# Performance work log

Hardware: AMD Instinct MI355X
Metric: run time of the kernel (lower is better)

The kernel has to match this reference:

```python
import jax, jax.numpy as jnp
import numpy as np
import math

B, C, H, W = 16, 512, 32, 32
GROUPS = 32
EPS = 1e-5


def group_norm(x, w, b):
    # x: [B, C, H, W]; normalize within each of GROUPS channel groups over (C//G, H, W)
    Bx, Cx, Hx, Wx = x.shape
    xg = x.reshape(Bx, GROUPS, Cx // GROUPS, Hx, Wx)
    mean = xg.mean(axis=(2, 3, 4), keepdims=True)
    var = xg.var(axis=(2, 3, 4), keepdims=True)
    xg = (xg - mean) * jax.lax.rsqrt(var + EPS)
    xn = xg.reshape(Bx, Cx, Hx, Wx)
    return xn * w[None, :, None, None] + b[None, :, None, None]


def setup_inputs() -> dict:
    key = jax.random.key(0)
    ks = jax.random.split(key, 4)
    x = jax.random.normal(ks[0], (B, C, H, W), dtype=jnp.float32)
    gn_w = jnp.ones((C,), dtype=jnp.float32)
    gn_b = jnp.zeros((C,), dtype=jnp.float32)
    # Conv2d 1x1 weights as [out, in] matrices; PyTorch default init scale
    qkv_w = jax.random.normal(ks[1], (3 * C, C), dtype=jnp.float32) * (1.0 / math.sqrt(C))
    qkv_b = jnp.zeros((3 * C,), dtype=jnp.float32)
    out_w = jax.random.normal(ks[2], (C, C), dtype=jnp.float32) * (1.0 / math.sqrt(C))
    out_b = jnp.zeros((C,), dtype=jnp.float32)
    return {"x": x, "gn_w": gn_w, "gn_b": gn_b, "qkv_w": qkv_w,
            "qkv_b": qkv_b, "out_w": out_w, "out_b": out_b}


def reference(x, gn_w, gn_b, qkv_w, qkv_b, out_w, out_b):
    Bx, Cx, Hx, Wx = x.shape
    N = Hx * Wx
    h = group_norm(x, gn_w, gn_b)                       # [B, C, H, W]
    hf = h.reshape(Bx, Cx, N)                           # [B, C, N]
    # 1x1 conv == channel matmul
    qkv = jnp.einsum('oc,bcn->bon', qkv_w, hf) + qkv_b[None, :, None]  # [B, 3C, N]
    q, k, v = jnp.split(qkv, 3, axis=1)                 # each [B, C, N]
    q = q.transpose(0, 2, 1)                            # [B, N, C]
    v = v.transpose(0, 2, 1)                            # [B, N, C]
    scale = 1.0 / math.sqrt(Cx)
    attn = jnp.einsum('bnc,bcm->bnm', q, k) * scale     # [B, N, N]
    attn = jax.nn.softmax(attn, axis=-1)
    o = jnp.einsum('bnm,bmc->bnc', attn, v)             # [B, N, C]
    o = o.transpose(0, 2, 1)                            # [B, C, N]
    o = jnp.einsum('oc,bcn->bon', out_w, o) + out_b[None, :, None]
    return x + o.reshape(Bx, Cx, Hx, Wx)
```

## Files before the change

### kernel.cpp

```cpp
#include <hip/hip_runtime.h>

typedef unsigned short u16;
typedef short short8 __attribute__((ext_vector_type(8)));
typedef float floatx4 __attribute__((ext_vector_type(4)));
typedef u16 u16x4 __attribute__((ext_vector_type(4)));
typedef u16 u16x8 __attribute__((ext_vector_type(8)));

#define DEVI __device__ __forceinline__

DEVI u16 f2bf(float x) {
    union { float f; unsigned u; } c; c.f = x;
    unsigned u = c.u;
    u += 0x7fffu + ((u >> 16) & 1u);
    return (u16)(u >> 16);
}
DEVI float bf2f(u16 h) {
    union { unsigned u; float f; } c; c.u = ((unsigned)h) << 16;
    return c.f;
}

DEVI void gload_lds16(const void* g, void* l) {
    auto gp = (const __attribute__((address_space(1))) unsigned*)(unsigned long long)g;
    auto lp = (__attribute__((address_space(3))) unsigned*)(unsigned)(unsigned long long)l;
    __builtin_amdgcn_global_load_lds(gp, lp, 16, 0, 0);
}

__global__ __launch_bounds__(256) void gn_fused_kernel(const float* __restrict__ x,
                                                       const float* __restrict__ w,
                                                       const float* __restrict__ bb,
                                                       u16* __restrict__ h) {
    const int bg = blockIdx.x;
    const int b = bg >> 5, g = bg & 31;
    const float* xg = x + (long long)bg * 16384;
    const int n0 = threadIdx.x * 4;

    float4 xv[16];
    float s = 0.f, s2 = 0.f;
    #pragma unroll
    for (int cc = 0; cc < 16; cc++) {
        xv[cc] = *(const float4*)&xg[cc * 1024 + n0];
        s  += xv[cc].x + xv[cc].y + xv[cc].z + xv[cc].w;
        s2 += xv[cc].x*xv[cc].x + xv[cc].y*xv[cc].y + xv[cc].z*xv[cc].z + xv[cc].w*xv[cc].w;
    }
    #pragma unroll
    for (int m = 1; m < 64; m <<= 1) { s += __shfl_xor(s, m, 64); s2 += __shfl_xor(s2, m, 64); }
    __shared__ float rs[4], rq[4];
    if ((threadIdx.x & 63) == 0) { rs[threadIdx.x >> 6] = s; rq[threadIdx.x >> 6] = s2; }
    __syncthreads();
    float mean = (rs[0] + rs[1] + rs[2] + rs[3]) * (1.f / 16384.f);
    float var  = (rq[0] + rq[1] + rq[2] + rq[3]) * (1.f / 16384.f) - mean * mean;
    float rstd = rsqrtf(var + 1e-5f);

    u16x8 o[4][2];
    #pragma unroll
    for (int cc = 0; cc < 16; cc++) {
        int c = g * 16 + cc;
        float sc = w[c] * rstd;
        float sh = bb[c] - mean * sc;
        o[0][cc >> 3][cc & 7] = f2bf(xv[cc].x * sc + sh);
        o[1][cc >> 3][cc & 7] = f2bf(xv[cc].y * sc + sh);
        o[2][cc >> 3][cc & 7] = f2bf(xv[cc].z * sc + sh);
        o[3][cc >> 3][cc & 7] = f2bf(xv[cc].w * sc + sh);
    }
    u16* hb = h + ((long long)b * 1024 + n0) * 512 + g * 16;
    #pragma unroll
    for (int k = 0; k < 4; k++) {
        *(u16x8*)&hb[(long long)k * 512]     = o[k][0];
        *(u16x8*)&hb[(long long)k * 512 + 8] = o[k][1];
    }
}

__global__ __launch_bounds__(256) void prep_kernel(const float* __restrict__ qkv_w, u16* __restrict__ wqb,
                                                   const float* __restrict__ out_w, u16* __restrict__ wob,
                                                   u16* __restrict__ wvT,
                                                   const float* __restrict__ qkv_b, float* __restrict__ dv) {
    const int bid = blockIdx.x;
    const int t = threadIdx.x;
    if (bid < 768) {
        int i = bid * 256 + t;
        const float* src; u16* dst; int j;
        if (i < 131072) { src = qkv_w; dst = wqb; j = i; }
        else            { src = out_w; dst = wob; j = i - 131072; }
        float4 v = *(const float4*)&src[j * 4];
        u16x4 p; p[0] = f2bf(v.x); p[1] = f2bf(v.y); p[2] = f2bf(v.z); p[3] = f2bf(v.w);
        *(u16x4*)&dst[j * 4] = p;
    } else if (bid < 784) {
        __shared__ u16 tile[128][132];
        const int tb = bid - 768;
        const int vbase = (tb >> 2) * 128, cbase = (tb & 3) * 128;
        #pragma unroll
        for (int rnd = 0; rnd < 16; rnd++) {
            int row = rnd * 8 + (t >> 5);
            int c4  = (t & 31) * 4;
            float4 v = *(const float4*)&qkv_w[(long long)(1024 + vbase + row) * 512 + cbase + c4];
            tile[row][c4 + 0] = f2bf(v.x);
            tile[row][c4 + 1] = f2bf(v.y);
            tile[row][c4 + 2] = f2bf(v.z);
            tile[row][c4 + 3] = f2bf(v.w);
        }
        __syncthreads();
        #pragma unroll
        for (int rnd = 0; rnd < 8; rnd++) {
            int r  = rnd * 16 + (t >> 4);
            int ch = (t & 15) * 8;
            u16x8 o;
            #pragma unroll
            for (int e = 0; e < 8; e++) o[e] = tile[ch + e][r];
            *(u16x8*)&wvT[(long long)(cbase + r) * 512 + vbase + ch] = o;
        }
    } else {
        int o = (bid - 784) * 256 + t;
        const float4* r = (const float4*)(out_w + (long long)o * 512);
        const float4* b = (const float4*)(qkv_b + 1024);
        float s = 0.f;
        #pragma unroll 4
        for (int c = 0; c < 128; c++) {
            float4 a = r[c], q = b[c];
            s += a.x*q.x + a.y*q.y + a.z*q.z + a.w*q.w;
        }
        dv[o] = s;
    }
}

__global__ __launch_bounds__(256) void lreduce_kernel(const float* __restrict__ ps,
                                                      float* __restrict__ invl) {
    int i = blockIdx.x * 256 + threadIdx.x;
    int z = i >> 10, n = i & 1023;
    float l = 0.f;
    #pragma unroll
    for (int kb = 0; kb < 8; kb++) l += ps[((z * 8 + kb) << 10) + n];
    invl[i] = 1.f / l;
}

template <int MODE, int NX, int NY, bool STATS>
__global__ __launch_bounds__(256, 4)
void gemm_bt_kernel(const u16* __restrict__ A, const u16* __restrict__ Bt,
                    void* __restrict__ C0,
                    const float* __restrict__ bias, const float* __restrict__ res,
                    float* __restrict__ aux,
                    float scale, int lda, int ldb, int ldc,
                    long long sA, long long sB, long long sC, long long sR, int K) {
    int bx, by, bz;
    if (NX > 0) {
        const int lid  = blockIdx.x;
        const int xcd  = lid & 7;
        const int slot = lid >> 3;
        const int per  = NX * NY;
        const int j    = slot / per;
        const int w    = slot - j * per;
        bz = xcd + 8 * j;
        bx = w % NX;
        by = w / NX;
    } else {
        bx = blockIdx.x; by = blockIdx.y; bz = blockIdx.z;
    }
    const int t    = threadIdx.x;
    const int lane = t & 63;
    const int wave = t >> 6;
    const int m0   = by * 128;
    const int n0   = bx * 128;
    A  += (long long)bz * sA;
    Bt += (long long)bz * sB;

    __shared__ __align__(16) u16 smem[16384];
    u16* As = smem;
    u16* Bs = smem + 8192;

    const int wm = wave >> 1, wn = wave & 1;
    const int quad = lane >> 4, lrow = lane & 15;

    floatx4 acc[4][4];
    #pragma unroll
    for (int i = 0; i < 4; i++)
        #pragma unroll
        for (int j = 0; j < 4; j++)
            #pragma unroll
            for (int r = 0; r < 4; r++) acc[i][j][r] = 0.f;

    const int rowA = t >> 2;
    const int kch  = (t & 3) * 8;
    const u16* Ag = A  + (long long)(m0 + rowA) * lda + kch;
    const u16* Bg = Bt + (long long)(n0 + rowA) * ldb + kch;
    u16* Al = &As[t * 8];
    u16* Bl = &Bs[t * 8];
    const long long a64 = (long long)64 * lda;
    const long long b64 = (long long)64 * ldb;

    for (int k0 = 0; k0 < K; k0 += 64) {
        gload_lds16(Ag + k0,            Al);
        gload_lds16(Ag + k0 + a64,      Al + 2048);
        gload_lds16(Ag + k0 + 32,       Al + 4096);
        gload_lds16(Ag + k0 + 32 + a64, Al + 6144);
        gload_lds16(Bg + k0,            Bl);
        gload_lds16(Bg + k0 + b64,      Bl + 2048);
        gload_lds16(Bg + k0 + 32,       Bl + 4096);
        gload_lds16(Bg + k0 + 32 + b64, Bl + 6144);
        __syncthreads();
        #pragma unroll
        for (int kk = 0; kk < 2; kk++) {
            short8 af[4], bfr[4];
            #pragma unroll
            for (int i = 0; i < 4; i++)
                af[i] = *(const short8*)&As[kk*4096 + (wm*64 + i*16 + lrow)*32 + quad*8];
            #pragma unroll
            for (int j = 0; j < 4; j++)
                bfr[j] = *(const short8*)&Bs[kk*4096 + (wn*64 + j*16 + lrow)*32 + quad*8];
            #pragma unroll
            for (int i = 0; i < 4; i++)
                #pragma unroll
                for (int j = 0; j < 4; j++)
                    acc[i][j] = __builtin_amdgcn_mfma_f32_16x16x32_bf16(af[i], bfr[j], acc[i][j], 0, 0, 0);
        }
        __syncthreads();
    }

    const int ST = 136;

    if (MODE == 1) {
        #pragma unroll
        for (int p = 0; p < 4; p++) {
            if (p) __syncthreads();
            if (wm == (p >> 1)) {
                #pragma unroll
                for (int ii = 0; ii < 2; ii++) {
                    const int i = (p & 1) * 2 + ii;
                    const int row = ii * 16 + quad * 4;
                    #pragma unroll
                    for (int j = 0; j < 4; j++) {
                        const int cB = wn * 64 + j * 16 + lrow;
                        #pragma unroll
                        for (int r = 0; r < 4; r++) {
                            float v = acc[i][j][r] * scale;
                            if (STATS) v = __expf(v);
                            else if (bias) v += bias[m0 + p * 32 + row + r];
                            smem[(row + r) * ST + cB] = f2bf(v);
                        }
                    }
                }
            }
            __syncthreads();
            const int rr = t >> 3, cc = (t & 7) * 16;
            u16x8 a0 = *(u16x8*)&smem[rr * ST + cc];
            u16x8 a1 = *(u16x8*)&smem[rr * ST + cc + 8];
            u16* Cp = (u16*)C0 + (long long)bz * sC + (long long)(m0 + p * 32 + rr) * ldc + n0 + cc;
            *(u16x8*)Cp = a0;
            *(u16x8*)(Cp + 8) = a1;
            if (STATS) {
                float ls = 0.f;
                #pragma unroll
                for (int e = 0; e < 8; e++)
                    ls += bf2f(a0[e]) + bf2f(a1[e]);
                #pragma unroll
                for (int m2 = 1; m2 < 8; m2 <<= 1) ls += __shfl_xor(ls, m2, 8);
                if ((t & 7) == 0)
                    aux[((long long)(bz * 8 + bx)) * 1024 + m0 + p * 32 + rr] = ls;
            }
        }
    } else if (MODE == 2) {
        #pragma unroll
        for (int p = 0; p < 4; p++) {
            if (p) __syncthreads();
            if (wn == (p >> 1)) {
                #pragma unroll
                for (int jj = 0; jj < 2; jj++) {
                    const int j = (p & 1) * 2 + jj;
                    const int row = jj * 16 + lrow;
                    #pragma unroll
                    for (int i = 0; i < 4; i++) {
                        const int mmL = wm * 64 + i * 16 + quad * 4;
                        u16x4 pk;
                        #pragma unroll
                        for (int r = 0; r < 4; r++)
                            pk[r] = f2bf(acc[i][j][r] + bias[m0 + mmL + r]);
                        *(u16x4*)&smem[row * ST + mmL] = pk;
                    }
                }
            }
            __syncthreads();
            const int rr = t >> 3, cc = (t & 7) * 16;
            u16x8 a0 = *(u16x8*)&smem[rr * ST + cc];
            u16x8 a1 = *(u16x8*)&smem[rr * ST + cc + 8];
            u16* Cp = (u16*)C0 + (long long)(n0 + p * 32 + rr) * ldc + m0 + cc;
            *(u16x8*)Cp = a0;
            *(u16x8*)(Cp + 8) = a1;
        }
    } else {
        float* smf = (float*)smem;
        const int SF = 132;
        float* C = (float*)C0 + (long long)bz * sC;
        const float* rz = res + (long long)bz * sR;
        const float* il = aux + (long long)bz * 1024;
        #pragma unroll
        for (int p = 0; p < 8; p++) {
            if (p) __syncthreads();
            if (wm == (p >> 2)) {
                const int i = p & 3;
                #pragma unroll
                for (int j = 0; j < 4; j++) {
                    const int cB = wn * 64 + j * 16 + lrow;
                    #pragma unroll
                    for (int r = 0; r < 4; r++)
                        smf[(quad * 4 + r) * SF + cB] = acc[i][j][r];
                }
            }
            __syncthreads();
            const int rr = t >> 4, cc = (t & 15) * 8;
            const float bsv = bias[m0 + p * 16 + rr];
            float4 il0 = *(const float4*)&il[n0 + cc];
            float4 il1 = *(const float4*)&il[n0 + cc + 4];
            const long long gro = (long long)(m0 + p * 16 + rr) * ldc + n0 + cc;
            float4 rv0 = *(const float4*)&rz[gro];
            float4 rv1 = *(const float4*)&rz[gro + 4];
            float4 ov0, ov1;
            ov0.x = smf[rr*SF + cc + 0] * il0.x + bsv + rv0.x;
            ov0.y = smf[rr*SF + cc + 1] * il0.y + bsv + rv0.y;
            ov0.z = smf[rr*SF + cc + 2] * il0.z + bsv + rv0.z;
            ov0.w = smf[rr*SF + cc + 3] * il0.w + bsv + rv0.w;
            ov1.x = smf[rr*SF + cc + 4] * il1.x + bsv + rv1.x;
            ov1.y = smf[rr*SF + cc + 5] * il1.y + bsv + rv1.y;
            ov1.z = smf[rr*SF + cc + 6] * il1.z + bsv + rv1.z;
            ov1.w = smf[rr*SF + cc + 7] * il1.w + bsv + rv1.w;
            *(float4*)&C[gro]     = ov0;
            *(float4*)&C[gro + 4] = ov1;
        }
    }
}

extern "C" void kernel_launch(void* const* d_in, const int* in_sizes, int n_in,
                              void* d_out, int out_size, void* d_ws, size_t ws_size,
                              hipStream_t stream) {
    (void)in_sizes; (void)n_in; (void)out_size; (void)ws_size;
    const float* x     = (const float*)d_in[0];
    const float* gn_w  = (const float*)d_in[1];
    const float* gn_b  = (const float*)d_in[2];
    const float* qkv_w = (const float*)d_in[3];
    const float* qkv_b = (const float*)d_in[4];
    const float* out_w = (const float*)d_in[5];
    const float* out_b = (const float*)d_in[6];
    float* out = (float*)d_out;

    char* ws = (char*)d_ws;
    u16*  h_t   = (u16*)ws;  ws += (size_t)16*1024*512*2;
    u16*  qkv_t = (u16*)ws;  ws += (size_t)16*1024*1024*2;
    u16*  vprm  = (u16*)ws;  ws += (size_t)512*16384*2;
    u16*  E     = (u16*)ws;  ws += (size_t)16*1024*1024*2;
    u16*  wqb   = (u16*)ws;  ws += (size_t)1024*512*2;
    u16*  wob   = (u16*)ws;  ws += (size_t)512*512*2;
    u16*  wvT   = (u16*)ws;  ws += (size_t)512*512*2;
    u16*  wprm  = (u16*)ws;  ws += (size_t)512*512*2;
    float* dv   = (float*)ws; ws += (size_t)512*4;
    float* psum = (float*)ws; ws += (size_t)16*8*1024*4;
    float* invl = (float*)ws; ws += (size_t)16*1024*4;

    prep_kernel<<<786, 256, 0, stream>>>(qkv_w, wqb, out_w, wob, wvT, qkv_b, dv);
    gn_fused_kernel<<<512, 256, 0, stream>>>(x, gn_w, gn_b, h_t);

    gemm_bt_kernel<1, 0, 0, false><<<dim3(4, 4, 1), 256, 0, stream>>>(
        wob, wvT, wprm, nullptr, nullptr, nullptr, 1.0f,
        512, 512, 512, 0, 0, 0, 0, 512);

    gemm_bt_kernel<2, 0, 0, false><<<dim3(128, 8, 1), 256, 0, stream>>>(
        wqb, h_t, qkv_t, qkv_b, nullptr, nullptr, 1.0f,
        512, 512, 1024, 0, 0, 0, 0, 512);

    gemm_bt_kernel<1, 0, 0, false><<<dim3(128, 4, 1), 256, 0, stream>>>(
        wprm, h_t, vprm, dv, nullptr, nullptr, 1.0f,
        512, 512, 16384, 0, 0, 0, 0, 512);

    gemm_bt_kernel<1, 8, 8, true><<<1024, 256, 0, stream>>>(
        qkv_t, qkv_t + 512, E, nullptr, nullptr, psum, 0.044194173824159216f,
        1024, 1024, 1024,
        (long long)1024*1024, (long long)1024*1024, (long long)1024*1024, 0, 512);

    lreduce_kernel<<<64, 256, 0, stream>>>(psum, invl);

    gemm_bt_kernel<3, 8, 4, false><<<512, 256, 0, stream>>>(
        vprm, E, out, out_b, x, invl, 1.0f,
        16384, 1024, 1024,
        1024, (long long)1024*1024, (long long)512*1024, (long long)512*1024, 1024);
}
```

Before: 234.0 us.

## Pad workspace leading dimensions and merge prep, groupnorm and weight-fold launches

Leading dimensions of the intermediate bf16 buffers (h, qkv, vprm, E) are padded beyond powers of two. The aim is to avoid partition and channel conflicts in global memory and cache for the strided GEMM loads. The groupnorm kernel is merged into the weight-prep kernel, and the small out_w×W_v fold GEMM rides in extra blocks of the QKV GEMM launch, cutting the launch count. The XCD-aware block swizzle is dropped in favour of plain 3D grids, and launch bounds drop from 4 to 3 blocks per CU. That could lose L2 locality and occupancy in exchange for more registers.

```diff
diff --git a/kernel.cpp b/kernel.cpp
--- a/kernel.cpp
+++ b/kernel.cpp
@@ -8,6 +8,10 @@
 
 #define DEVI __device__ __forceinline__
 
+#define LDH 544
+#define LDQ 1088
+#define LDV 16448
+
 DEVI u16 f2bf(float x) {
     union { float f; unsigned u; } c; c.f = x;
     unsigned u = c.u;
@@ -25,68 +29,66 @@
     __builtin_amdgcn_global_load_lds(gp, lp, 16, 0, 0);
 }
 
-__global__ __launch_bounds__(256) void gn_fused_kernel(const float* __restrict__ x,
-                                                       const float* __restrict__ w,
-                                                       const float* __restrict__ bb,
-                                                       u16* __restrict__ h) {
-    const int bg = blockIdx.x;
-    const int b = bg >> 5, g = bg & 31;
-    const float* xg = x + (long long)bg * 16384;
-    const int n0 = threadIdx.x * 4;
-
-    float4 xv[16];
-    float s = 0.f, s2 = 0.f;
-    #pragma unroll
-    for (int cc = 0; cc < 16; cc++) {
-        xv[cc] = *(const float4*)&xg[cc * 1024 + n0];
-        s  += xv[cc].x + xv[cc].y + xv[cc].z + xv[cc].w;
-        s2 += xv[cc].x*xv[cc].x + xv[cc].y*xv[cc].y + xv[cc].z*xv[cc].z + xv[cc].w*xv[cc].w;
-    }
-    #pragma unroll
-    for (int m = 1; m < 64; m <<= 1) { s += __shfl_xor(s, m, 64); s2 += __shfl_xor(s2, m, 64); }
-    __shared__ float rs[4], rq[4];
-    if ((threadIdx.x & 63) == 0) { rs[threadIdx.x >> 6] = s; rq[threadIdx.x >> 6] = s2; }
-    __syncthreads();
-    float mean = (rs[0] + rs[1] + rs[2] + rs[3]) * (1.f / 16384.f);
-    float var  = (rq[0] + rq[1] + rq[2] + rq[3]) * (1.f / 16384.f) - mean * mean;
-    float rstd = rsqrtf(var + 1e-5f);
-
-    u16x8 o[4][2];
-    #pragma unroll
-    for (int cc = 0; cc < 16; cc++) {
-        int c = g * 16 + cc;
-        float sc = w[c] * rstd;
-        float sh = bb[c] - mean * sc;
-        o[0][cc >> 3][cc & 7] = f2bf(xv[cc].x * sc + sh);
-        o[1][cc >> 3][cc & 7] = f2bf(xv[cc].y * sc + sh);
-        o[2][cc >> 3][cc & 7] = f2bf(xv[cc].z * sc + sh);
-        o[3][cc >> 3][cc & 7] = f2bf(xv[cc].w * sc + sh);
-    }
-    u16* hb = h + ((long long)b * 1024 + n0) * 512 + g * 16;
-    #pragma unroll
-    for (int k = 0; k < 4; k++) {
-        *(u16x8*)&hb[(long long)k * 512]     = o[k][0];
-        *(u16x8*)&hb[(long long)k * 512 + 8] = o[k][1];
-    }
-}
-
-__global__ __launch_bounds__(256) void prep_kernel(const float* __restrict__ qkv_w, u16* __restrict__ wqb,
-                                                   const float* __restrict__ out_w, u16* __restrict__ wob,
-                                                   u16* __restrict__ wvT,
-                                                   const float* __restrict__ qkv_b, float* __restrict__ dv) {
+__global__ __launch_bounds__(256) void prepgn_kernel(const float* __restrict__ x,
+                                                     const float* __restrict__ gw,
+                                                     const float* __restrict__ gb,
+                                                     u16* __restrict__ h,
+                                                     const float* __restrict__ qkv_w, u16* __restrict__ wqb,
+                                                     const float* __restrict__ out_w, u16* __restrict__ wob,
+                                                     u16* __restrict__ wvT,
+                                                     const float* __restrict__ qkv_b, float* __restrict__ dv) {
     const int bid = blockIdx.x;
     const int t = threadIdx.x;
-    if (bid < 768) {
-        int i = bid * 256 + t;
+    if (bid < 512) {
+        const int b = bid >> 5, g = bid & 31;
+        const float* xg = x + (long long)bid * 16384;
+        const int n0 = t * 4;
+
+        float4 xv[16];
+        float s = 0.f, s2 = 0.f;
+        #pragma unroll
+        for (int cc = 0; cc < 16; cc++) {
+            xv[cc] = *(const float4*)&xg[cc * 1024 + n0];
+            s  += xv[cc].x + xv[cc].y + xv[cc].z + xv[cc].w;
+            s2 += xv[cc].x*xv[cc].x + xv[cc].y*xv[cc].y + xv[cc].z*xv[cc].z + xv[cc].w*xv[cc].w;
+        }
+        #pragma unroll
+        for (int m = 1; m < 64; m <<= 1) { s += __shfl_xor(s, m, 64); s2 += __shfl_xor(s2, m, 64); }
+        __shared__ float rs[4], rq[4];
+        if ((t & 63) == 0) { rs[t >> 6] = s; rq[t >> 6] = s2; }
+        __syncthreads();
+        float mean = (rs[0] + rs[1] + rs[2] + rs[3]) * (1.f / 16384.f);
+        float var  = (rq[0] + rq[1] + rq[2] + rq[3]) * (1.f / 16384.f) - mean * mean;
+        float rstd = rsqrtf(var + 1e-5f);
+
+        u16x8 o[4][2];
+        #pragma unroll
+        for (int cc = 0; cc < 16; cc++) {
+            int c = g * 16 + cc;
+            float sc = gw[c] * rstd;
+            float sh = gb[c] - mean * sc;
+            o[0][cc >> 3][cc & 7] = f2bf(xv[cc].x * sc + sh);
+            o[1][cc >> 3][cc & 7] = f2bf(xv[cc].y * sc + sh);
+            o[2][cc >> 3][cc & 7] = f2bf(xv[cc].z * sc + sh);
+            o[3][cc >> 3][cc & 7] = f2bf(xv[cc].w * sc + sh);
+        }
+        u16* hb = h + ((long long)b * 1024 + n0) * LDH + g * 16;
+        #pragma unroll
+        for (int k = 0; k < 4; k++) {
+            *(u16x8*)&hb[(long long)k * LDH]     = o[k][0];
+            *(u16x8*)&hb[(long long)k * LDH + 8] = o[k][1];
+        }
+    } else if (bid < 1280) {
+        int i = (bid - 512) * 256 + t;
         const float* src; u16* dst; int j;
         if (i < 131072) { src = qkv_w; dst = wqb; j = i; }
         else            { src = out_w; dst = wob; j = i - 131072; }
         float4 v = *(const float4*)&src[j * 4];
         u16x4 p; p[0] = f2bf(v.x); p[1] = f2bf(v.y); p[2] = f2bf(v.z); p[3] = f2bf(v.w);
         *(u16x4*)&dst[j * 4] = p;
-    } else if (bid < 784) {
+    } else if (bid < 1296) {
         __shared__ u16 tile[128][132];
-        const int tb = bid - 768;
+        const int tb = bid - 1280;
         const int vbase = (tb >> 2) * 128, cbase = (tb & 3) * 128;
         #pragma unroll
         for (int rnd = 0; rnd < 16; rnd++) {
@@ -109,7 +111,7 @@
             *(u16x8*)&wvT[(long long)(cbase + r) * 512 + vbase + ch] = o;
         }
     } else {
-        int o = (bid - 784) * 256 + t;
+        int o = (bid - 1296) * 256 + t;
         const float4* r = (const float4*)(out_w + (long long)o * 512);
         const float4* b = (const float4*)(qkv_b + 1024);
         float s = 0.f;
@@ -132,35 +134,35 @@
     invl[i] = 1.f / l;
 }
 
-template <int MODE, int NX, int NY, bool STATS>
-__global__ __launch_bounds__(256, 4)
+template <int MODE, bool STATS, bool FOLDW>
+__global__ __launch_bounds__(256, 3)
 void gemm_bt_kernel(const u16* __restrict__ A, const u16* __restrict__ Bt,
                     void* __restrict__ C0,
                     const float* __restrict__ bias, const float* __restrict__ res,
                     float* __restrict__ aux,
+                    const u16* __restrict__ A2, const u16* __restrict__ B2, u16* __restrict__ C2,
                     float scale, int lda, int ldb, int ldc,
                     long long sA, long long sB, long long sC, long long sR, int K) {
-    int bx, by, bz;
-    if (NX > 0) {
-        const int lid  = blockIdx.x;
-        const int xcd  = lid & 7;
-        const int slot = lid >> 3;
-        const int per  = NX * NY;
-        const int j    = slot / per;
-        const int w    = slot - j * per;
-        bz = xcd + 8 * j;
-        bx = w % NX;
-        by = w / NX;
-    } else {
-        bx = blockIdx.x; by = blockIdx.y; bz = blockIdx.z;
+    int bx = blockIdx.x, by = blockIdx.y;
+    const int bz = blockIdx.z;
+    bool isW = false;
+    int ldA = lda, ldB = ldb, ldC = ldc;
+    const u16* Ap = A;
+    const u16* Bp = Bt;
+    if (FOLDW && bx >= 128) {
+        isW = true;
+        const int tb = (bx - 128) * 8 + by;
+        bx = tb & 3; by = tb >> 2;
+        Ap = A2; Bp = B2;
+        ldA = 512; ldB = 512; ldC = 512;
     }
     const int t    = threadIdx.x;
     const int lane = t & 63;
     const int wave = t >> 6;
     const int m0   = by * 128;
     const int n0   = bx * 128;
-    A  += (long long)bz * sA;
-    Bt += (long long)bz * sB;
+    Ap += (long long)bz * sA;
+    Bp += (long long)bz * sB;
 
     __shared__ __align__(16) u16 smem[16384];
     u16* As = smem;
@@ -179,12 +181,12 @@
 
     const int rowA = t >> 2;
     const int kch  = (t & 3) * 8;
-    const u16* Ag = A  + (long long)(m0 + rowA) * lda + kch;
-    const u16* Bg = Bt + (long long)(n0 + rowA) * ldb + kch;
+    const u16* Ag = Ap + (long long)(m0 + rowA) * ldA + kch;
+    const u16* Bg = Bp + (long long)(n0 + rowA) * ldB + kch;
     u16* Al = &As[t * 8];
     u16* Bl = &Bs[t * 8];
-    const long long a64 = (long long)64 * lda;
-    const long long b64 = (long long)64 * ldb;
+    const long long a64 = (long long)64 * ldA;
+    const long long b64 = (long long)64 * ldB;
 
     for (int k0 = 0; k0 < K; k0 += 64) {
         gload_lds16(Ag + k0,            Al);
@@ -216,7 +218,8 @@
 
     const int ST = 136;
 
-    if (MODE == 1) {
+    if (MODE == 1 || isW) {
+        u16* Cbase = isW ? C2 : (u16*)C0;
         #pragma unroll
         for (int p = 0; p < 4; p++) {
             if (p) __syncthreads();
@@ -232,7 +235,7 @@
                         for (int r = 0; r < 4; r++) {
                             float v = acc[i][j][r] * scale;
                             if (STATS) v = __expf(v);
-                            else if (bias) v += bias[m0 + p * 32 + row + r];
+                            else if (!isW && bias) v += bias[m0 + p * 32 + row + r];
                             smem[(row + r) * ST + cB] = f2bf(v);
                         }
                     }
@@ -242,7 +245,7 @@
             const int rr = t >> 3, cc = (t & 7) * 16;
             u16x8 a0 = *(u16x8*)&smem[rr * ST + cc];
             u16x8 a1 = *(u16x8*)&smem[rr * ST + cc + 8];
-            u16* Cp = (u16*)C0 + (long long)bz * sC + (long long)(m0 + p * 32 + rr) * ldc + n0 + cc;
+            u16* Cp = Cbase + (long long)bz * sC + (long long)(m0 + p * 32 + rr) * ldC + n0 + cc;
             *(u16x8*)Cp = a0;
             *(u16x8*)(Cp + 8) = a1;
             if (STATS) {
@@ -280,7 +283,7 @@
             const int rr = t >> 3, cc = (t & 7) * 16;
             u16x8 a0 = *(u16x8*)&smem[rr * ST + cc];
             u16x8 a1 = *(u16x8*)&smem[rr * ST + cc + 8];
-            u16* Cp = (u16*)C0 + (long long)(n0 + p * 32 + rr) * ldc + m0 + cc;
+            u16* Cp = (u16*)C0 + (long long)(n0 + p * 32 + rr) * ldC + m0 + cc;
             *(u16x8*)Cp = a0;
             *(u16x8*)(Cp + 8) = a1;
         }
@@ -308,7 +311,7 @@
             const float bsv = bias[m0 + p * 16 + rr];
             float4 il0 = *(const float4*)&il[n0 + cc];
             float4 il1 = *(const float4*)&il[n0 + cc + 4];
-            const long long gro = (long long)(m0 + p * 16 + rr) * ldc + n0 + cc;
+            const long long gro = (long long)(m0 + p * 16 + rr) * ldC + n0 + cc;
             float4 rv0 = *(const float4*)&rz[gro];
             float4 rv1 = *(const float4*)&rz[gro + 4];
             float4 ov0, ov1;
@@ -340,10 +343,10 @@
     float* out = (float*)d_out;
 
     char* ws = (char*)d_ws;
-    u16*  h_t   = (u16*)ws;  ws += (size_t)16*1024*512*2;
-    u16*  qkv_t = (u16*)ws;  ws += (size_t)16*1024*1024*2;
-    u16*  vprm  = (u16*)ws;  ws += (size_t)512*16384*2;
-    u16*  E     = (u16*)ws;  ws += (size_t)16*1024*1024*2;
+    u16*  h_t   = (u16*)ws;  ws += (size_t)16*1024*LDH*2;
+    u16*  qkv_t = (u16*)ws;  ws += (size_t)16*1024*LDQ*2;
+    u16*  vprm  = (u16*)ws;  ws += (size_t)512*LDV*2;
+    u16*  E     = (u16*)ws;  ws += (size_t)16*1024*LDQ*2;
     u16*  wqb   = (u16*)ws;  ws += (size_t)1024*512*2;
     u16*  wob   = (u16*)ws;  ws += (size_t)512*512*2;
     u16*  wvT   = (u16*)ws;  ws += (size_t)512*512*2;
@@ -352,30 +355,30 @@
     float* psum = (float*)ws; ws += (size_t)16*8*1024*4;
     float* invl = (float*)ws; ws += (size_t)16*1024*4;
 
-    prep_kernel<<<786, 256, 0, stream>>>(qkv_w, wqb, out_w, wob, wvT, qkv_b, dv);
-    gn_fused_kernel<<<512, 256, 0, stream>>>(x, gn_w, gn_b, h_t);
-
-    gemm_bt_kernel<1, 0, 0, false><<<dim3(4, 4, 1), 256, 0, stream>>>(
-        wob, wvT, wprm, nullptr, nullptr, nullptr, 1.0f,
-        512, 512, 512, 0, 0, 0, 0, 512);
-
-    gemm_bt_kernel<2, 0, 0, false><<<dim3(128, 8, 1), 256, 0, stream>>>(
-        wqb, h_t, qkv_t, qkv_b, nullptr, nullptr, 1.0f,
-        512, 512, 1024, 0, 0, 0, 0, 512);
-
-    gemm_bt_kernel<1, 0, 0, false><<<dim3(128, 4, 1), 256, 0, stream>>>(
-        wprm, h_t, vprm, dv, nullptr, nullptr, 1.0f,
-        512, 512, 16384, 0, 0, 0, 0, 512);
-
-    gemm_bt_kernel<1, 8, 8, true><<<1024, 256, 0, stream>>>(
-        qkv_t, qkv_t + 512, E, nullptr, nullptr, psum, 0.044194173824159216f,
-        1024, 1024, 1024,
-        (long long)1024*1024, (long long)1024*1024, (long long)1024*1024, 0, 512);
+    prepgn_kernel<<<1298, 256, 0, stream>>>(x, gn_w, gn_b, h_t,
+                                            qkv_w, wqb, out_w, wob, wvT, qkv_b, dv);
+
+    gemm_bt_kernel<2, false, true><<<dim3(130, 8, 1), 256, 0, stream>>>(
+        wqb, h_t, qkv_t, qkv_b, nullptr, nullptr,
+        wob, wvT, wprm, 1.0f,
+        512, LDH, LDQ, 0, 0, 0, 0, 512);
+
+    gemm_bt_kernel<1, false, false><<<dim3(128, 4, 1), 256, 0, stream>>>(
+        wprm, h_t, vprm, dv, nullptr, nullptr,
+        nullptr, nullptr, nullptr, 1.0f,
+        512, LDH, LDV, 0, 0, 0, 0, 512);
+
+    gemm_bt_kernel<1, true, false><<<dim3(8, 8, 16), 256, 0, stream>>>(
+        qkv_t, qkv_t + 512, E, nullptr, nullptr, psum,
+        nullptr, nullptr, nullptr, 0.044194173824159216f,
+        LDQ, LDQ, LDQ,
+        (long long)1024*LDQ, (long long)1024*LDQ, (long long)1024*LDQ, 0, 512);
 
     lreduce_kernel<<<64, 256, 0, stream>>>(psum, invl);
 
-    gemm_bt_kernel<3, 8, 4, false><<<512, 256, 0, stream>>>(
-        vprm, E, out, out_b, x, invl, 1.0f,
-        16384, 1024, 1024,
-        1024, (long long)1024*1024, (long long)512*1024, (long long)512*1024, 1024);
-}
+    gemm_bt_kernel<3, false, false><<<dim3(8, 4, 16), 256, 0, stream>>>(
+        vprm, E, out, out_b, x, invl,
+        nullptr, nullptr, nullptr, 1.0f,
+        LDV, LDQ, 1024,
+        1024, (long long)1024*LDQ, (long long)512*1024, (long long)512*1024, 1024);
+}
```

Result: slower. 247.7 us (+5.9%).
